# Kernel tuning notes

Hardware: AMD Instinct MI355X
Metric: run time of the kernel (lower is better)

The kernel has to match this reference:

```python
import jax, jax.numpy as jnp
import numpy as np

B, S, D = 16, 2048, 128

def setup_inputs() -> dict:
    key = jax.random.key(0)
    kq, kk, kv = jax.random.split(key, 3)
    return {
        "query": jax.random.normal(kq, (B, S, D), dtype=jnp.float32),
        "key": jax.random.normal(kk, (B, S, D), dtype=jnp.float32),
        "value": jax.random.normal(kv, (B, S, D), dtype=jnp.float32),
    }

def reference(query, key, value):
    # query: (B, S2, d), key: (B, S1, d), value: (B, S1, d)
    d_k = query.shape[-1]
    scale = 1.0 / jnp.sqrt(jnp.asarray(d_k, dtype=query.dtype))
    # (B, S2, S1) attention scores
    att = jnp.einsum('bqd,bkd->bqk', query, key) * scale
    att = jax.nn.softmax(att, axis=-1)
    # (B, S2, d_v)
    return jnp.einsum('bqk,bkd->bqd', att, value)
```

## Files before the change

### kernel.cpp

```cpp
#include <hip/hip_runtime.h>
#include <hip/hip_bf16.h>

#define B_N 16
#define S_LEN 2048
#define D_DIM 128
#define TK 32
#define NTH 32

typedef __attribute__((ext_vector_type(16))) float f32x16;
typedef __attribute__((ext_vector_type(8)))  short short8;
typedef const __attribute__((address_space(1))) void* gp1;
typedef __attribute__((address_space(3))) void* sp3;
#define GLL(g, l) __builtin_amdgcn_global_load_lds((gp1)(const void*)(g), (sp3)(void*)(l), 16, 0, 0)

static __device__ __forceinline__ unsigned short f2bf(float f) {
  unsigned u = __builtin_bit_cast(unsigned, f);
  return (unsigned short)((u + 0x7fffu + ((u >> 16) & 1u)) >> 16);
}

static __device__ __forceinline__ unsigned pk_bf16(float a, float b) {
#if __has_builtin(__builtin_amdgcn_cvt_pk_bf16_f32)
  typedef __attribute__((ext_vector_type(2))) __bf16 bf16x2;
  bf16x2 r = __builtin_amdgcn_cvt_pk_bf16_f32(a, b);
  return __builtin_bit_cast(unsigned, r);
#else
  return (unsigned)f2bf(a) | ((unsigned)f2bf(b) << 16);
#endif
}

__global__ __launch_bounds__(256)
void prep_kernel(const float* __restrict__ K, const float* __restrict__ V,
                 unsigned short* __restrict__ Kb, unsigned short* __restrict__ VT) {
  __shared__ unsigned short lds[64 * 66];
  int bx = blockIdx.x;
  int t  = threadIdx.x;
  if (bx < 4096) {
    size_t i = ((size_t)bx * 256 + t) * 4;
    float4 v = *(const float4*)(K + i);
    *(uint2*)(Kb + i) = make_uint2(pk_bf16(v.x, v.y), pk_bf16(v.z, v.w));
  } else {
    int bi = bx - 4096;
    int b  = bi & 15;
    int st = (bi >> 4) & 31;
    int dt = bi >> 9;
    const float* Vb = V + ((size_t)b * S_LEN + st * 64) * D_DIM + dt * 64;
    unsigned short* VTb = VT + ((size_t)b * D_DIM + dt * 64) * S_LEN + st * 64;
#pragma unroll
    for (int rep = 0; rep < 4; ++rep) {
      int idx = rep * 256 + t;
      int i  = idx >> 4;
      int j4 = (idx & 15) * 4;
      float4 v = *(const float4*)(Vb + (size_t)i * D_DIM + j4);
      *(uint2*)&lds[i * 66 + j4] = make_uint2(pk_bf16(v.x, v.y), pk_bf16(v.z, v.w));
    }
    __syncthreads();
#pragma unroll
    for (int rep = 0; rep < 4; ++rep) {
      int idx = rep * 256 + t;
      int dd = idx >> 4;
      int s4 = (idx & 15) * 4;
      unsigned short e0 = lds[(s4 + 0) * 66 + dd];
      unsigned short e1 = lds[(s4 + 1) * 66 + dd];
      unsigned short e2 = lds[(s4 + 2) * 66 + dd];
      unsigned short e3 = lds[(s4 + 3) * 66 + dd];
      *(uint2*)(VTb + (size_t)dd * S_LEN + s4) =
          make_uint2((unsigned)e0 | ((unsigned)e1 << 16),
                     (unsigned)e2 | ((unsigned)e3 << 16));
    }
  }
}

__global__ __launch_bounds__(512, 2)
void attn_kernel(const float* __restrict__ Q, const unsigned short* __restrict__ Kb,
                 const unsigned short* __restrict__ VT, float* __restrict__ O) {
  __shared__ __align__(16) char smem[66048];

  const int tid  = threadIdx.x;
  const int wave = tid >> 6;
  const int g    = wave >> 2;
  const int w4   = wave & 3;
  const int lane = tid & 63;
  const int l32  = lane & 31;
  const int half = lane >> 5;

  const int i     = blockIdx.x;
  const int b     = (i & 7) * 2 + ((i >> 3) & 1);
  const int qtile = i >> 4;
  const int qbase = qtile * 128 + w4 * 32;

  const float* Qb = Q + (size_t)b * S_LEN * D_DIM;
  const unsigned short* Kbb = Kb + (size_t)b * S_LEN * D_DIM;
  const unsigned short* VTb = VT + (size_t)b * D_DIM * S_LEN;

  unsigned short* kb0 = (unsigned short*)smem + g * 8192;
  unsigned short* vb0 = (unsigned short*)(smem + 32768) + g * 8192;

  const unsigned short* kgp[2];
  const unsigned short* vgp[2];
  unsigned short* kdst[2][2];
  unsigned short* vdst[2][2];
#pragma unroll
  for (int cc = 0; cc < 2; ++cc) {
    int c  = w4 * 2 + cc;
    int rl = 4 * c + (lane >> 4);
    int lbk = (lane & 15) ^ (rl & 15);
    kgp[cc] = Kbb + (size_t)(g * NTH * TK + rl) * D_DIM + lbk * 8;
    int dv = 16 * c + (lane >> 2);
    int lbv = (lane & 3) ^ ((dv >> 1) & 3);
    vgp[cc] = VTb + (size_t)dv * S_LEN + g * NTH * TK + lbv * 8;
    kdst[0][cc] = kb0 + c * 512;  kdst[1][cc] = kb0 + 4096 + c * 512;
    vdst[0][cc] = vb0 + c * 512;  vdst[1][cc] = vb0 + 4096 + c * 512;
  }
#pragma unroll
  for (int cc = 0; cc < 2; ++cc) { GLL(kgp[cc], kdst[0][cc]); GLL(vgp[cc], vdst[0][cc]); }

  int kOff[8], vOff[8];
#pragma unroll
  for (int ks = 0; ks < 8; ++ks)
    kOff[ks] = (l32 * D_DIM + (((ks << 1) + half) ^ (l32 & 15)) * 8) * 2;
#pragma unroll
  for (int ks2 = 0; ks2 < 2; ++ks2)
#pragma unroll
    for (int dt = 0; dt < 4; ++dt) {
      int dv = dt * 32 + l32;
      int pv = ((ks2 << 1) + half) ^ ((dv >> 1) & 3);
      vOff[ks2 * 4 + dt] = (dv * TK + pv * 8) * 2;
    }

  const float SC = 0.08838834764831845f * 1.4426950408889634f;
  short8 qa[8];
  {
    const float* qp = Qb + (size_t)(qbase + l32) * D_DIM + half * 8;
#pragma unroll
    for (int ks = 0; ks < 8; ++ks) {
      float4 a0 = *(const float4*)(qp + ks * 16);
      float4 a1 = *(const float4*)(qp + ks * 16 + 4);
      union { unsigned u[4]; short8 s; } pu;
      pu.u[0] = pk_bf16(a0.x * SC, a0.y * SC);
      pu.u[1] = pk_bf16(a0.z * SC, a0.w * SC);
      pu.u[2] = pk_bf16(a1.x * SC, a1.y * SC);
      pu.u[3] = pk_bf16(a1.z * SC, a1.w * SC);
      qa[ks] = pu.s;
    }
  }

  const f32x16 zf16 = {0.f,0.f,0.f,0.f,0.f,0.f,0.f,0.f,0.f,0.f,0.f,0.f,0.f,0.f,0.f,0.f};
  f32x16 oacc[4];
#pragma unroll
  for (int dt = 0; dt < 4; ++dt) oacc[dt] = zf16;
  float lp[4] = {0.f, 0.f, 0.f, 0.f};

  for (int t = 0; t < NTH; ++t) {
    __syncthreads();
    const int cb = t & 1;
    const char* kbc = (const char*)kb0 + cb * 8192;
    const char* vbc = (const char*)vb0 + cb * 8192;

    if (t + 1 < NTH) {
      const int nb = cb ^ 1;
#pragma unroll
      for (int cc = 0; cc < 2; ++cc) {
        kgp[cc] += TK * D_DIM;  GLL(kgp[cc], kdst[nb][cc]);
        vgp[cc] += TK;          GLL(vgp[cc], vdst[nb][cc]);
      }
    }

    f32x16 sacc = zf16;
#pragma unroll
    for (int ks = 0; ks < 8; ++ks) {
      short8 kf = *(const short8*)(kbc + kOff[ks]);
      sacc = __builtin_amdgcn_mfma_f32_32x32x16_bf16(kf, qa[ks], sacc, 0, 0, 0);
    }

    float p[16];
#pragma unroll
    for (int r = 0; r < 16; ++r) p[r] = exp2f(sacc[r]);
#pragma unroll
    for (int r = 0; r < 16; ++r) lp[r & 3] += p[r];
    unsigned w[8];
#pragma unroll
    for (int j = 0; j < 8; ++j) w[j] = pk_bf16(p[2 * j], p[2 * j + 1]);

#pragma unroll
    for (int ks2 = 0; ks2 < 2; ++ks2) {
      const int a = ks2 * 4;
      unsigned x0 = (unsigned)__shfl_xor((int)w[a + 0], 32);
      unsigned x1 = (unsigned)__shfl_xor((int)w[a + 1], 32);
      unsigned x2 = (unsigned)__shfl_xor((int)w[a + 2], 32);
      unsigned x3 = (unsigned)__shfl_xor((int)w[a + 3], 32);
      union { unsigned u[4]; short8 s; } pu;
      pu.u[0] = half ? x2 : w[a + 0];
      pu.u[1] = half ? x3 : w[a + 1];
      pu.u[2] = half ? w[a + 2] : x0;
      pu.u[3] = half ? w[a + 3] : x1;
      short8 pf = pu.s;
#pragma unroll
      for (int dt = 0; dt < 4; ++dt) {
        short8 vf = *(const short8*)(vbc + vOff[ks2 * 4 + dt]);
        oacc[dt] = __builtin_amdgcn_mfma_f32_32x32x16_bf16(pf, vf, oacc[dt], 0, 0, 0);
      }
    }
  }

  float lt = (lp[0] + lp[1]) + (lp[2] + lp[3]);
  lt += __shfl_xor(lt, 32);

  __syncthreads();
  float* mo = (float*)(smem + w4 * 16512);
  float* ml = (float*)(smem + w4 * 16512 + 16384);
  if (g == 1) {
#pragma unroll
    for (int reg = 0; reg < 16; ++reg) {
      int row = (reg & 3) + 8 * (reg >> 2) + 4 * half;
#pragma unroll
      for (int dt = 0; dt < 4; ++dt)
        mo[row * 128 + dt * 32 + l32] = oacc[dt][reg];
    }
    if (half == 0) ml[l32] = lt;
  }
  __syncthreads();
  if (g == 0) {
    float tot = lt + ml[l32];
    float* Ob = O + (size_t)b * S_LEN * D_DIM;
#pragma unroll
    for (int reg = 0; reg < 16; ++reg) {
      int row = (reg & 3) + 8 * (reg >> 2) + 4 * half;
      float linv = 1.f / __shfl(tot, row);
#pragma unroll
      for (int dt = 0; dt < 4; ++dt)
        Ob[(size_t)(qbase + row) * D_DIM + dt * 32 + l32] =
            (oacc[dt][reg] + mo[row * 128 + dt * 32 + l32]) * linv;
    }
  }
}

extern "C" void kernel_launch(void* const* d_in, const int* in_sizes, int n_in,
                              void* d_out, int out_size, void* d_ws, size_t ws_size,
                              hipStream_t stream) {
  const float* Q = (const float*)d_in[0];
  const float* K = (const float*)d_in[1];
  const float* V = (const float*)d_in[2];
  float* O = (float*)d_out;
  unsigned short* Kb = (unsigned short*)d_ws;
  unsigned short* VT = Kb + (size_t)B_N * S_LEN * D_DIM;
  prep_kernel<<<dim3(4096 + 1024), dim3(256), 0, stream>>>(K, V, Kb, VT);
  attn_kernel<<<dim3(256), dim3(512), 0, stream>>>(Q, Kb, VT, O);
}
```

Before: 149.3 us.

## Split attention key range across three wave groups per block

Each block grows from 512 to 768 threads. The key sequence is split over three groups of waves (22/21/21 tiles of 32 keys) instead of two, so each wave runs fewer serial key-loop iterations. With 256 blocks over 256 CUs, this raises the number of waves active per CU. LDS use roughly doubles to hold the extra K/V buffers and the reduction slots. The final merge now sums two partial outputs and row sums per query group. The larger LDS footprint and 3-waves-per-SIMD launch bound limit occupancy and the register budget.

Result: no change. 148.1 us (-0.8%).

```diff
diff --git a/kernel.cpp b/kernel.cpp
--- a/kernel.cpp
+++ b/kernel.cpp
@@ -5,7 +5,6 @@
 #define S_LEN 2048
 #define D_DIM 128
 #define TK 32
-#define NTH 32
 
 typedef __attribute__((ext_vector_type(16))) float f32x16;
 typedef __attribute__((ext_vector_type(8)))  short short8;
@@ -70,30 +69,33 @@
   }
 }
 
-__global__ __launch_bounds__(512, 2)
+__global__ __launch_bounds__(768, 3)
 void attn_kernel(const float* __restrict__ Q, const unsigned short* __restrict__ Kb,
                  const unsigned short* __restrict__ VT, float* __restrict__ O) {
-  __shared__ __align__(16) char smem[66048];
+  __shared__ __align__(16) char smem[132096];
 
   const int tid  = threadIdx.x;
   const int wave = tid >> 6;
-  const int g    = wave >> 2;
-  const int w4   = wave & 3;
+  const int qg   = wave & 3;
+  const int kg   = wave >> 2;
   const int lane = tid & 63;
   const int l32  = lane & 31;
   const int half = lane >> 5;
 
+  const int NK  = (kg == 0) ? 22 : 21;
+  const int KB0 = (kg == 0) ? 0 : 704 + (kg - 1) * 672;
+
   const int i     = blockIdx.x;
   const int b     = (i & 7) * 2 + ((i >> 3) & 1);
   const int qtile = i >> 4;
-  const int qbase = qtile * 128 + w4 * 32;
+  const int qbase = qtile * 128 + qg * 32;
 
   const float* Qb = Q + (size_t)b * S_LEN * D_DIM;
   const unsigned short* Kbb = Kb + (size_t)b * S_LEN * D_DIM;
   const unsigned short* VTb = VT + (size_t)b * D_DIM * S_LEN;
 
-  unsigned short* kb0 = (unsigned short*)smem + g * 8192;
-  unsigned short* vb0 = (unsigned short*)(smem + 32768) + g * 8192;
+  char* kbase = smem + kg * 16384;
+  char* vbase = smem + 49152 + kg * 16384;
 
   const unsigned short* kgp[2];
   const unsigned short* vgp[2];
@@ -101,15 +103,17 @@
   unsigned short* vdst[2][2];
 #pragma unroll
   for (int cc = 0; cc < 2; ++cc) {
-    int c  = w4 * 2 + cc;
+    int c  = qg * 2 + cc;
     int rl = 4 * c + (lane >> 4);
     int lbk = (lane & 15) ^ (rl & 15);
-    kgp[cc] = Kbb + (size_t)(g * NTH * TK + rl) * D_DIM + lbk * 8;
+    kgp[cc] = Kbb + (size_t)(KB0 + rl) * D_DIM + lbk * 8;
     int dv = 16 * c + (lane >> 2);
     int lbv = (lane & 3) ^ ((dv >> 1) & 3);
-    vgp[cc] = VTb + (size_t)dv * S_LEN + g * NTH * TK + lbv * 8;
-    kdst[0][cc] = kb0 + c * 512;  kdst[1][cc] = kb0 + 4096 + c * 512;
-    vdst[0][cc] = vb0 + c * 512;  vdst[1][cc] = vb0 + 4096 + c * 512;
+    vgp[cc] = VTb + (size_t)dv * S_LEN + KB0 + lbv * 8;
+    kdst[0][cc] = (unsigned short*)kbase + c * 512;
+    kdst[1][cc] = (unsigned short*)(kbase + 8192) + c * 512;
+    vdst[0][cc] = (unsigned short*)vbase + c * 512;
+    vdst[1][cc] = (unsigned short*)(vbase + 8192) + c * 512;
   }
 #pragma unroll
   for (int cc = 0; cc < 2; ++cc) { GLL(kgp[cc], kdst[0][cc]); GLL(vgp[cc], vdst[0][cc]); }
@@ -150,13 +154,13 @@
   for (int dt = 0; dt < 4; ++dt) oacc[dt] = zf16;
   float lp[4] = {0.f, 0.f, 0.f, 0.f};
 
-  for (int t = 0; t < NTH; ++t) {
+  for (int t = 0; t < 22; ++t) {
     __syncthreads();
     const int cb = t & 1;
-    const char* kbc = (const char*)kb0 + cb * 8192;
-    const char* vbc = (const char*)vb0 + cb * 8192;
-
-    if (t + 1 < NTH) {
+    const char* kbc = kbase + cb * 8192;
+    const char* vbc = vbase + cb * 8192;
+
+    if (t + 1 < NK) {
       const int nb = cb ^ 1;
 #pragma unroll
       for (int cc = 0; cc < 2; ++cc) {
@@ -165,39 +169,41 @@
       }
     }
 
-    f32x16 sacc = zf16;
-#pragma unroll
-    for (int ks = 0; ks < 8; ++ks) {
-      short8 kf = *(const short8*)(kbc + kOff[ks]);
-      sacc = __builtin_amdgcn_mfma_f32_32x32x16_bf16(kf, qa[ks], sacc, 0, 0, 0);
-    }
-
-    float p[16];
-#pragma unroll
-    for (int r = 0; r < 16; ++r) p[r] = exp2f(sacc[r]);
-#pragma unroll
-    for (int r = 0; r < 16; ++r) lp[r & 3] += p[r];
-    unsigned w[8];
-#pragma unroll
-    for (int j = 0; j < 8; ++j) w[j] = pk_bf16(p[2 * j], p[2 * j + 1]);
-
-#pragma unroll
-    for (int ks2 = 0; ks2 < 2; ++ks2) {
-      const int a = ks2 * 4;
-      unsigned x0 = (unsigned)__shfl_xor((int)w[a + 0], 32);
-      unsigned x1 = (unsigned)__shfl_xor((int)w[a + 1], 32);
-      unsigned x2 = (unsigned)__shfl_xor((int)w[a + 2], 32);
-      unsigned x3 = (unsigned)__shfl_xor((int)w[a + 3], 32);
-      union { unsigned u[4]; short8 s; } pu;
-      pu.u[0] = half ? x2 : w[a + 0];
-      pu.u[1] = half ? x3 : w[a + 1];
-      pu.u[2] = half ? w[a + 2] : x0;
-      pu.u[3] = half ? w[a + 3] : x1;
-      short8 pf = pu.s;
-#pragma unroll
-      for (int dt = 0; dt < 4; ++dt) {
-        short8 vf = *(const short8*)(vbc + vOff[ks2 * 4 + dt]);
-        oacc[dt] = __builtin_amdgcn_mfma_f32_32x32x16_bf16(pf, vf, oacc[dt], 0, 0, 0);
+    if (t < NK) {
+      f32x16 sacc = zf16;
+#pragma unroll
+      for (int ks = 0; ks < 8; ++ks) {
+        short8 kf = *(const short8*)(kbc + kOff[ks]);
+        sacc = __builtin_amdgcn_mfma_f32_32x32x16_bf16(kf, qa[ks], sacc, 0, 0, 0);
+      }
+
+      float p[16];
+#pragma unroll
+      for (int r = 0; r < 16; ++r) p[r] = exp2f(sacc[r]);
+#pragma unroll
+      for (int r = 0; r < 16; ++r) lp[r & 3] += p[r];
+      unsigned w[8];
+#pragma unroll
+      for (int j = 0; j < 8; ++j) w[j] = pk_bf16(p[2 * j], p[2 * j + 1]);
+
+#pragma unroll
+      for (int ks2 = 0; ks2 < 2; ++ks2) {
+        const int a = ks2 * 4;
+        unsigned x0 = (unsigned)__shfl_xor((int)w[a + 0], 32);
+        unsigned x1 = (unsigned)__shfl_xor((int)w[a + 1], 32);
+        unsigned x2 = (unsigned)__shfl_xor((int)w[a + 2], 32);
+        unsigned x3 = (unsigned)__shfl_xor((int)w[a + 3], 32);
+        union { unsigned u[4]; short8 s; } pu;
+        pu.u[0] = half ? x2 : w[a + 0];
+        pu.u[1] = half ? x3 : w[a + 1];
+        pu.u[2] = half ? w[a + 2] : x0;
+        pu.u[3] = half ? w[a + 3] : x1;
+        short8 pf = pu.s;
+#pragma unroll
+        for (int dt = 0; dt < 4; ++dt) {
+          short8 vf = *(const short8*)(vbc + vOff[ks2 * 4 + dt]);
+          oacc[dt] = __builtin_amdgcn_mfma_f32_32x32x16_bf16(pf, vf, oacc[dt], 0, 0, 0);
+        }
       }
     }
   }
@@ -206,30 +212,36 @@
   lt += __shfl_xor(lt, 32);
 
   __syncthreads();
-  float* mo = (float*)(smem + w4 * 16512);
-  float* ml = (float*)(smem + w4 * 16512 + 16384);
-  if (g == 1) {
+  float* oslot = (float*)smem;
+  float* larr  = (float*)(smem + 131072);
+  if (kg > 0) {
+    const int s = qg * 2 + (kg - 1);
+    float* os = oslot + s * 4096;
 #pragma unroll
     for (int reg = 0; reg < 16; ++reg) {
       int row = (reg & 3) + 8 * (reg >> 2) + 4 * half;
 #pragma unroll
       for (int dt = 0; dt < 4; ++dt)
-        mo[row * 128 + dt * 32 + l32] = oacc[dt][reg];
-    }
-    if (half == 0) ml[l32] = lt;
+        os[row * 128 + dt * 32 + l32] = oacc[dt][reg];
+    }
+    if (half == 0) larr[s * 32 + l32] = lt;
   }
   __syncthreads();
-  if (g == 0) {
-    float tot = lt + ml[l32];
+  if (kg == 0) {
+    const float* os0 = oslot + (qg * 2 + 0) * 4096;
+    const float* os1 = oslot + (qg * 2 + 1) * 4096;
+    float tot = lt + larr[(qg * 2 + 0) * 32 + l32] + larr[(qg * 2 + 1) * 32 + l32];
     float* Ob = O + (size_t)b * S_LEN * D_DIM;
 #pragma unroll
     for (int reg = 0; reg < 16; ++reg) {
       int row = (reg & 3) + 8 * (reg >> 2) + 4 * half;
       float linv = 1.f / __shfl(tot, row);
 #pragma unroll
-      for (int dt = 0; dt < 4; ++dt)
+      for (int dt = 0; dt < 4; ++dt) {
+        int cix = row * 128 + dt * 32 + l32;
         Ob[(size_t)(qbase + row) * D_DIM + dt * 32 + l32] =
-            (oacc[dt][reg] + mo[row * 128 + dt * 32 + l32]) * linv;
+            (oacc[dt][reg] + os0[cix] + os1[cix]) * linv;
+      }
     }
   }
 }
@@ -244,5 +256,5 @@
   unsigned short* Kb = (unsigned short*)d_ws;
   unsigned short* VT = Kb + (size_t)B_N * S_LEN * D_DIM;
   prep_kernel<<<dim3(4096 + 1024), dim3(256), 0, stream>>>(K, V, Kb, VT);
-  attn_kernel<<<dim3(256), dim3(512), 0, stream>>>(Q, Kb, VT, O);
-}
+  attn_kernel<<<dim3(256), dim3(768), 0, stream>>>(Q, Kb, VT, O);
+}
```

## Give each wave private K/V tiles and drop block barriers and split-KV merge

Applied to the files above, without the earlier changes.

The block shrinks from eight waves, split into two KV halves, to four waves that each walk the full key range. Each wave now streams its own private double-buffered K/V tiles into LDS and waits with explicit vmcnt waits instead of __syncthreads. This removes the per-iteration block barrier and the final LDS merge of the two partial outputs. The cost is four times the LDS fill traffic per block, twice the serial iterations per wave, fewer resident waves to hide latency, and 128KB of LDS per block.

New measurement: 176.7 us. 1.18x slower.

```diff
diff --git a/kernel.cpp b/kernel.cpp
--- a/kernel.cpp
+++ b/kernel.cpp
@@ -5,13 +5,16 @@
 #define S_LEN 2048
 #define D_DIM 128
 #define TK 32
-#define NTH 32
+#define NT (S_LEN / TK)
 
 typedef __attribute__((ext_vector_type(16))) float f32x16;
 typedef __attribute__((ext_vector_type(8)))  short short8;
 typedef const __attribute__((address_space(1))) void* gp1;
 typedef __attribute__((address_space(3))) void* sp3;
 #define GLL(g, l) __builtin_amdgcn_global_load_lds((gp1)(const void*)(g), (sp3)(void*)(l), 16, 0, 0)
+
+#define WAITCNT_VM16 0x4F70
+#define WAITCNT_VM0  0x0F70
 
 static __device__ __forceinline__ unsigned short f2bf(float f) {
   unsigned u = __builtin_bit_cast(unsigned, f);
@@ -70,15 +73,13 @@
   }
 }
 
-__global__ __launch_bounds__(512, 2)
+__global__ __launch_bounds__(256, 1)
 void attn_kernel(const float* __restrict__ Q, const unsigned short* __restrict__ Kb,
                  const unsigned short* __restrict__ VT, float* __restrict__ O) {
-  __shared__ __align__(16) char smem[66048];
+  __shared__ __align__(16) char smem[131072];
 
   const int tid  = threadIdx.x;
   const int wave = tid >> 6;
-  const int g    = wave >> 2;
-  const int w4   = wave & 3;
   const int lane = tid & 63;
   const int l32  = lane & 31;
   const int half = lane >> 5;
@@ -86,33 +87,31 @@
   const int i     = blockIdx.x;
   const int b     = (i & 7) * 2 + ((i >> 3) & 1);
   const int qtile = i >> 4;
-  const int qbase = qtile * 128 + w4 * 32;
+  const int qbase = qtile * 128 + wave * 32;
 
   const float* Qb = Q + (size_t)b * S_LEN * D_DIM;
   const unsigned short* Kbb = Kb + (size_t)b * S_LEN * D_DIM;
   const unsigned short* VTb = VT + (size_t)b * D_DIM * S_LEN;
 
-  unsigned short* kb0 = (unsigned short*)smem + g * 8192;
-  unsigned short* vb0 = (unsigned short*)(smem + 32768) + g * 8192;
-
-  const unsigned short* kgp[2];
-  const unsigned short* vgp[2];
-  unsigned short* kdst[2][2];
-  unsigned short* vdst[2][2];
-#pragma unroll
-  for (int cc = 0; cc < 2; ++cc) {
-    int c  = w4 * 2 + cc;
-    int rl = 4 * c + (lane >> 4);
+  char* kbase = smem + wave * 32768;
+  char* vbase = kbase + 16384;
+
+  unsigned kGo[8], vGo[8];
+#pragma unroll
+  for (int c = 0; c < 8; ++c) {
+    int rl  = 4 * c + (lane >> 4);
     int lbk = (lane & 15) ^ (rl & 15);
-    kgp[cc] = Kbb + (size_t)(g * NTH * TK + rl) * D_DIM + lbk * 8;
-    int dv = 16 * c + (lane >> 2);
+    kGo[c] = (unsigned)(rl * D_DIM + lbk * 8);
+    int dv  = 16 * c + (lane >> 2);
     int lbv = (lane & 3) ^ ((dv >> 1) & 3);
-    vgp[cc] = VTb + (size_t)dv * S_LEN + g * NTH * TK + lbv * 8;
-    kdst[0][cc] = kb0 + c * 512;  kdst[1][cc] = kb0 + 4096 + c * 512;
-    vdst[0][cc] = vb0 + c * 512;  vdst[1][cc] = vb0 + 4096 + c * 512;
-  }
-#pragma unroll
-  for (int cc = 0; cc < 2; ++cc) { GLL(kgp[cc], kdst[0][cc]); GLL(vgp[cc], vdst[0][cc]); }
+    vGo[c] = (unsigned)(dv * S_LEN + lbv * 8);
+  }
+
+#pragma unroll
+  for (int c = 0; c < 8; ++c) {
+    GLL(Kbb + kGo[c], kbase + c * 1024);
+    GLL(VTb + vGo[c], vbase + c * 1024);
+  }
 
   int kOff[8], vOff[8];
 #pragma unroll
@@ -150,19 +149,23 @@
   for (int dt = 0; dt < 4; ++dt) oacc[dt] = zf16;
   float lp[4] = {0.f, 0.f, 0.f, 0.f};
 
-  for (int t = 0; t < NTH; ++t) {
-    __syncthreads();
+  for (int t = 0; t < NT; ++t) {
     const int cb = t & 1;
-    const char* kbc = (const char*)kb0 + cb * 8192;
-    const char* vbc = (const char*)vb0 + cb * 8192;
-
-    if (t + 1 < NTH) {
+    const char* kbc = kbase + cb * 8192;
+    const char* vbc = vbase + cb * 8192;
+
+    if (t + 1 < NT) {
       const int nb = cb ^ 1;
-#pragma unroll
-      for (int cc = 0; cc < 2; ++cc) {
-        kgp[cc] += TK * D_DIM;  GLL(kgp[cc], kdst[nb][cc]);
-        vgp[cc] += TK;          GLL(vgp[cc], vdst[nb][cc]);
+      const unsigned short* kt = Kbb + (size_t)(t + 1) * TK * D_DIM;
+      const unsigned short* vt = VTb + (size_t)(t + 1) * TK;
+#pragma unroll
+      for (int c = 0; c < 8; ++c) {
+        GLL(kt + kGo[c], kbase + nb * 8192 + c * 1024);
+        GLL(vt + vGo[c], vbase + nb * 8192 + c * 1024);
       }
+      __builtin_amdgcn_s_waitcnt(WAITCNT_VM16);
+    } else {
+      __builtin_amdgcn_s_waitcnt(WAITCNT_VM0);
     }
 
     f32x16 sacc = zf16;
@@ -205,32 +208,14 @@
   float lt = (lp[0] + lp[1]) + (lp[2] + lp[3]);
   lt += __shfl_xor(lt, 32);
 
-  __syncthreads();
-  float* mo = (float*)(smem + w4 * 16512);
-  float* ml = (float*)(smem + w4 * 16512 + 16384);
-  if (g == 1) {
-#pragma unroll
-    for (int reg = 0; reg < 16; ++reg) {
-      int row = (reg & 3) + 8 * (reg >> 2) + 4 * half;
-#pragma unroll
-      for (int dt = 0; dt < 4; ++dt)
-        mo[row * 128 + dt * 32 + l32] = oacc[dt][reg];
-    }
-    if (half == 0) ml[l32] = lt;
-  }
-  __syncthreads();
-  if (g == 0) {
-    float tot = lt + ml[l32];
-    float* Ob = O + (size_t)b * S_LEN * D_DIM;
-#pragma unroll
-    for (int reg = 0; reg < 16; ++reg) {
-      int row = (reg & 3) + 8 * (reg >> 2) + 4 * half;
-      float linv = 1.f / __shfl(tot, row);
-#pragma unroll
-      for (int dt = 0; dt < 4; ++dt)
-        Ob[(size_t)(qbase + row) * D_DIM + dt * 32 + l32] =
-            (oacc[dt][reg] + mo[row * 128 + dt * 32 + l32]) * linv;
-    }
+  float* Ob = O + (size_t)b * S_LEN * D_DIM;
+#pragma unroll
+  for (int reg = 0; reg < 16; ++reg) {
+    int row = (reg & 3) + 8 * (reg >> 2) + 4 * half;
+    float linv = 1.f / __shfl(lt, row);
+#pragma unroll
+    for (int dt = 0; dt < 4; ++dt)
+      Ob[(size_t)(qbase + row) * D_DIM + dt * 32 + l32] = oacc[dt][reg] * linv;
   }
 }
 
@@ -244,5 +229,5 @@
   unsigned short* Kb = (unsigned short*)d_ws;
   unsigned short* VT = Kb + (size_t)B_N * S_LEN * D_DIM;
   prep_kernel<<<dim3(4096 + 1024), dim3(256), 0, stream>>>(K, V, Kb, VT);
-  attn_kernel<<<dim3(256), dim3(512), 0, stream>>>(Q, Kb, VT, O);
-}
+  attn_kernel<<<dim3(256), dim3(256), 0, stream>>>(Q, Kb, VT, O);
+}
```
